# Kernel tuning notes

Hardware: AMD Instinct MI355X
Metric: run time of the kernel (lower is better)

The kernel has to match this reference:

```python
import jax, jax.numpy as jnp
import numpy as np

N = 20000      # num nodes
E = 320000     # num edges (avg degree 16)
R = 8          # num relations
D = 256        # input_dim / hidden dim
L = 6          # num_layers
EE = 32        # edge_embed_dim
B = 64         # batch size
K = 32         # num_negative + 1


def _layer_norm(x, g, b, eps=1e-5):
    mu = jnp.mean(x, axis=-1, keepdims=True)
    var = jnp.var(x, axis=-1, keepdims=True)
    return (x - mu) * jax.lax.rsqrt(var + eps) * g + b


def setup_inputs() -> dict:
    key = jax.random.key(0)
    ks = jax.random.split(key, 10)
    edge_index = jax.random.randint(ks[0], (2, E), 0, N)
    edge_type = jax.random.randint(ks[1], (E,), 0, R)
    edge_embed = jax.random.normal(ks[2], (E, EE), dtype=jnp.float32)
    src = jax.random.randint(ks[3], (B, K), 0, N)
    tgt = jax.random.randint(ks[4], (B, K), 0, N)
    rel = jax.random.randint(ks[5], (B, K), 0, R)
    batch = jnp.stack([src, tgt, rel], axis=-1)  # [B, K, 3]
    s = 1.0 / np.sqrt(D)
    W = jax.random.normal(ks[6], (L, R, D, D), dtype=jnp.float32) * s      # per-relation weights
    Wself = jax.random.normal(ks[7], (L, D, D), dtype=jnp.float32) * s     # self-loop weights
    We = jax.random.normal(ks[8], (L, EE, D), dtype=jnp.float32) * (1.0 / np.sqrt(EE))  # edge-embed proj (stage add)
    gamma = jnp.ones((L, D), dtype=jnp.float32)
    beta = jnp.zeros((L, D), dtype=jnp.float32)
    rel_emb = jax.random.normal(ks[9], (R, D), dtype=jnp.float32) * s      # DistMult relation embedding
    return dict(edge_index=edge_index, edge_type=edge_type, edge_embed=edge_embed,
                batch=batch, W=W, Wself=Wself, We=We, gamma=gamma, beta=beta,
                rel_emb=rel_emb)


def reference(edge_index, edge_type, edge_embed, batch, W, Wself, We, gamma, beta, rel_emb):
    src, dst = edge_index[0], edge_index[1]
    # mean aggregation denominator: in-degree per node (over all relations)
    deg = jnp.clip(jax.ops.segment_sum(jnp.ones((E,), jnp.float32), dst, num_segments=N), 1.0)
    # segment id combining relation and destination node -> aggregate-then-transform trick
    seg = edge_type * N + dst
    x = jnp.ones((N, D), dtype=jnp.float32)
    for l in range(L):
        # stage 'add': message = x[src] + proj(edge_embed)
        msg = x[src] + edge_embed @ We[l]                                  # [E, D]
        agg = jax.ops.segment_sum(msg, seg, num_segments=R * N).reshape(R, N, D)
        h = jnp.einsum('rnd,rdf->nf', agg, W[l]) / deg[:, None] + x @ Wself[l]
        h = jax.nn.relu(_layer_norm(h, gamma[l], beta[l]))
        x = h + x  # short_cut residual
    # DistMult scoring: gather source/target/relation embeddings, mul, sum
    s_emb = x[batch[..., 0]]          # [B, K, D]
    t_emb = x[batch[..., 1]]          # [B, K, D]
    r_emb = rel_emb[batch[..., 2]]    # [B, K, D]
    return jnp.sum(s_emb * r_emb * t_emb, axis=-1)  # [B, K]
```

## Files before the change

kernel.cpp:

```cpp
#include <hip/hip_runtime.h>
#include <hip/hip_bf16.h>

#define NN 20000
#define NP 20080
#define NE 320000
#define RR 8
#define DD 256
#define LL 6
#define EED 32
#define BB 64
#define KK 32
#define MM (NN * RR)
#define NSB 79
#define BMR 80
#define NGB 251

typedef __bf16 bf8 __attribute__((ext_vector_type(8)));
typedef float f4 __attribute__((ext_vector_type(4)));

__device__ inline float lo2f(unsigned v) { return __uint_as_float(v << 16); }
__device__ inline float hi2f(unsigned v) { return __uint_as_float(v & 0xffff0000u); }
__device__ inline unsigned short f2bf(float f) {
    unsigned u = __float_as_uint(f);
    return (unsigned short)((u + 0x7fff + ((u >> 16) & 1)) >> 16);
}
__device__ inline unsigned pack2(float lo, float hi) {
    return (unsigned)f2bf(lo) | ((unsigned)f2bf(hi) << 16);
}

#define GLOAD_LDS16(src, dst)                                                  \
    __builtin_amdgcn_global_load_lds(                                          \
        (const __attribute__((address_space(1))) unsigned int*)(src),          \
        (__attribute__((address_space(3))) unsigned int*)(dst), 16, 0, 0)


__global__ __launch_bounds__(256) void hist_kernel(const int* __restrict__ dstv,
                                                   const int* __restrict__ typev,
                                                   int* __restrict__ hist) {
    int e = blockIdx.x * 256 + threadIdx.x;
    if (e < NE) atomicAdd(&hist[dstv[e] * 8 + typev[e]], 1);
}

__global__ __launch_bounds__(256) void scan1_kernel(const int* __restrict__ hist,
                                                    int* __restrict__ excl,
                                                    int* __restrict__ bsums) {
    __shared__ int tmp[256];
    int tid = threadIdx.x;
    int base = blockIdx.x * 2048 + tid * 8;
    int v[8]; int s = 0;
#pragma unroll
    for (int i = 0; i < 8; ++i) {
        v[i] = (base + i < MM) ? hist[base + i] : 0;
        s += v[i];
    }
    tmp[tid] = s;
    __syncthreads();
    for (int off = 1; off < 256; off <<= 1) {
        int t = (tid >= off) ? tmp[tid - off] : 0;
        __syncthreads();
        tmp[tid] += t;
        __syncthreads();
    }
    int run = tmp[tid] - s;
#pragma unroll
    for (int i = 0; i < 8; ++i) {
        if (base + i < MM) excl[base + i] = run;
        run += v[i];
    }
    if (tid == 255) bsums[blockIdx.x] = tmp[255];
}

__global__ __launch_bounds__(128) void scan2_kernel(int* __restrict__ bsums) {
    __shared__ int tmp[128];
    int tid = threadIdx.x;
    int orig = (tid < NSB) ? bsums[tid] : 0;
    tmp[tid] = orig;
    __syncthreads();
    for (int off = 1; off < 128; off <<= 1) {
        int t = (tid >= off) ? tmp[tid - off] : 0;
        __syncthreads();
        tmp[tid] += t;
        __syncthreads();
    }
    if (tid < NSB) bsums[tid] = tmp[tid] - orig;
}

__global__ __launch_bounds__(256) void add_off_kernel(const int* __restrict__ excl,
                                                      const int* __restrict__ bsums,
                                                      int* __restrict__ seg_start,
                                                      int* __restrict__ cursor) {
    int i = blockIdx.x * 256 + threadIdx.x;
    if (i < MM) {
        int v = excl[i] + bsums[i >> 11];
        seg_start[i] = v;
        cursor[i] = v;
    }
    if (i == 0) seg_start[MM] = NE;
}

__global__ __launch_bounds__(256) void sort_scatter_kernel(
    const int* __restrict__ srcv, const int* __restrict__ dstv,
    const int* __restrict__ typev, int* __restrict__ cursor,
    int* __restrict__ esrc, int* __restrict__ eid) {
    int e = blockIdx.x * 256 + threadIdx.x;
    if (e < NE) {
        int key = dstv[e] * 8 + typev[e];
        int pos = atomicAdd(&cursor[key], 1);
        esrc[pos] = srcv[e];
        eid[pos]  = e;
    }
}

__global__ __launch_bounds__(256) void invdeg_kernel(const int* __restrict__ seg_start,
                                                     float* __restrict__ invdeg) {
    int i = blockIdx.x * 256 + threadIdx.x;
    if (i < NN) {
        int d = seg_start[i * 8 + 8] - seg_start[i * 8];
        invdeg[i] = 1.0f / (float)max(d, 1);
    }
}


__global__ __launch_bounds__(256) void eagg_kernel(
    const int* __restrict__ seg_start, const int* __restrict__ eid,
    const float* __restrict__ ee, const float* __restrict__ invdeg,
    unsigned short* __restrict__ eaggbf) {
    int tid = threadIdx.x;
    int s = blockIdx.x * 8 + (tid >> 5);
    int j = tid & 31;
    int n = s >> 3, r = s & 7;
    int j0 = seg_start[s], j1 = seg_start[s + 1];
    float sum = 0.0f;
    for (int p = j0; p < j1; ++p)
        sum += ee[eid[p] * EED + j];
    eaggbf[(size_t)n * DD + r * EED + j] = f2bf(sum * invdeg[n]);
}

__global__ __launch_bounds__(256) void whe_kernel(const float* __restrict__ We,
                                                  const float* __restrict__ W,
                                                  float* __restrict__ Whe) {
    __shared__ float WeS[EED * 32];
    int b = blockIdx.x;
    int l = b >> 6;
    int r = (b >> 3) & 7;
    int dc = b & 7;
    int tid = threadIdx.x;
    {
        int j = tid >> 3, dl = (tid & 7) * 4;
        *(float4*)&WeS[j * 32 + dl] =
            *(const float4*)&We[(size_t)l * EED * DD + (size_t)j * DD + dc * 32 + dl];
    }
    __syncthreads();
    const float* Wr = W + ((size_t)l * 8 + r) * DD * DD + (size_t)dc * 32 * DD;
    float acc[EED];
#pragma unroll
    for (int j = 0; j < EED; ++j) acc[j] = 0.0f;
    for (int dl = 0; dl < 32; ++dl) {
        float w = Wr[(size_t)dl * DD + tid];
#pragma unroll
        for (int j = 0; j < EED; ++j) acc[j] += WeS[j * 32 + dl] * w;
    }
    float* outp = Whe + (size_t)l * DD * DD + r * EED * DD + tid;
#pragma unroll
    for (int j = 0; j < EED; ++j) unsafeAtomicAdd(&outp[j * DD], acc[j]);
}

__global__ __launch_bounds__(256) void bswz_kernel(const float* __restrict__ W,
                                                   const float* __restrict__ Wself,
                                                   const float* __restrict__ Whe,
                                                   unsigned short* __restrict__ Bsw) {
    int gid = blockIdx.x * 256 + threadIdx.x;
    int f = gid & 255;
    int t = gid >> 8;
    int quad = t & 3; t >>= 2;
    int kb = t & 7; t >>= 3;
    int p = t % 10, l = t / 10;
    const float* base = (p == 0) ? Wself + (size_t)l * DD * DD
                      : (p <= 8) ? W + ((size_t)l * 8 + (p - 1)) * DD * DD
                                 : Whe + (size_t)l * DD * DD;
    int k0 = kb * 32 + quad * 8;
    unsigned pk[4];
#pragma unroll
    for (int jj = 0; jj < 4; ++jj)
        pk[jj] = pack2(base[(size_t)(k0 + 2 * jj) * DD + f],
                       base[(size_t)(k0 + 2 * jj + 1) * DD + f]);
    uint4 v = make_uint4(pk[0], pk[1], pk[2], pk[3]);
    *(uint4*)&Bsw[(size_t)gid * 8] = v;
}

__global__ __launch_bounds__(256) void init_x_kernel(float* __restrict__ x,
                                                     unsigned short* __restrict__ xbf) {
    int i = blockIdx.x * 256 + threadIdx.x;
    ((float4*)x)[i] = make_float4(1.f, 1.f, 1.f, 1.f);
    ((uint2*)xbf)[i] = make_uint2(0x3f803f80u, 0x3f803f80u);
}

__global__ __launch_bounds__(512) void agg_kernel(
    const int* __restrict__ seg_start, const int* __restrict__ esrc,
    const unsigned short* __restrict__ xbf, unsigned short* __restrict__ Abf) {
    int wv = threadIdx.x >> 6, lane = threadIdx.x & 63;
    int n = blockIdx.x * 8 + wv;
    if (n >= NN) return;
    int jb[9];
#pragma unroll
    for (int r = 0; r < 9; ++r) jb[r] = seg_start[n * 8 + r];
    float idg = 1.0f / (float)max(jb[8] - jb[0], 1);
    int cofs = lane * 4;
#pragma unroll
    for (int rr = 0; rr < 8; ++rr) {
        int j0 = jb[rr], j1 = jb[rr + 1];
        float a0 = 0.f, a1 = 0.f, a2 = 0.f, a3 = 0.f;
#pragma unroll 1
        for (int j = j0; j < j1; j += 8) {
            int rem = j1 - j;
            uint2 gvv[8];
#pragma unroll
            for (int t = 0; t < 8; ++t) {
                int jj = (t < rem) ? j + t : j;
                gvv[t] = *(const uint2*)&xbf[(size_t)esrc[jj] * DD + cofs];
            }
#pragma unroll
            for (int t = 0; t < 8; ++t) {
                unsigned vx = (t < rem) ? gvv[t].x : 0u;
                unsigned vy = (t < rem) ? gvv[t].y : 0u;
                a0 += lo2f(vx); a1 += hi2f(vx);
                a2 += lo2f(vy); a3 += hi2f(vy);
            }
        }
        *(uint2*)&Abf[(size_t)n * 2048 + rr * 256 + cofs] =
            make_uint2(pack2(a0 * idg, a1 * idg), pack2(a2 * idg, a3 * idg));
    }
}

__global__ __launch_bounds__(512) void gemm_layer_kernel(
    const unsigned short* __restrict__ xbfin, const unsigned short* __restrict__ Abf,
    const unsigned short* __restrict__ eaggbf, const unsigned short* __restrict__ Bswl,
    const float* __restrict__ xin, const float* __restrict__ gl,
    const float* __restrict__ bl, float* __restrict__ xout,
    unsigned short* __restrict__ xbfout) {
    __shared__ __align__(16) unsigned char smem[81920];
    int tid = threadIdx.x;
    int wv = tid >> 6, lane = tid & 63;
    int row0 = blockIdx.x * BMR;
    int m = lane & 15, quad = lane >> 4;
    f4 acc[5][2] = {};

#pragma unroll
    for (int i = 0; i < 5; ++i) {
        int bc = i * 512 + wv * 64;
        int c = bc + lane;
        int row = c >> 5, sc = c & 31, scs = sc ^ (row & 31);
        const unsigned short* src = xbfin + (size_t)(row0 + row) * DD + scs * 8;
        GLOAD_LDS16(src, smem + (size_t)bc * 16 + (size_t)lane * 16);
    }
    bf8 breg[2][2];
#pragma unroll
    for (int nt = 0; nt < 2; ++nt) {
        breg[0][nt] = *(const bf8*)&Bswl[((size_t)quad * 256 + wv * 32 + nt * 16 + m) * 8];
        breg[1][nt] = *(const bf8*)&Bswl[((size_t)(4 + quad) * 256 + wv * 32 + nt * 16 + m) * 8];
    }
    __syncthreads();

#pragma unroll 1
    for (int p = 0; p < 10; ++p) {
        unsigned char* bufp = smem + (p & 1) * 40960;
        unsigned char* bufn = smem + ((p + 1) & 1) * 40960;
        if (p < 9) {
            int q = p + 1;
            const unsigned short* sb;
            size_t rs;
            if (q <= 8) { sb = Abf + (size_t)row0 * 2048 + (size_t)(q - 1) * 256; rs = 2048; }
            else        { sb = eaggbf + (size_t)row0 * DD; rs = DD; }
#pragma unroll
            for (int i = 0; i < 5; ++i) {
                int bc = i * 512 + wv * 64;
                int c = bc + lane;
                int row = c >> 5, sc = c & 31, scs = sc ^ (row & 31);
                const unsigned short* src = sb + (size_t)row * rs + scs * 8;
                GLOAD_LDS16(src, bufn + (size_t)bc * 16 + (size_t)lane * 16);
            }
        }
#pragma unroll
        for (int kb = 0; kb < 8; ++kb) {
            bf8 afr[5];
#pragma unroll
            for (int mt = 0; mt < 5; ++mt) {
                int rowl = mt * 16 + m;
                afr[mt] = *(bf8*)&bufp[rowl * 512 + (((kb * 4 + quad) ^ (rowl & 31)) * 16)];
            }
#pragma unroll
            for (int mt = 0; mt < 5; ++mt)
#pragma unroll
                for (int nt = 0; nt < 2; ++nt)
                    acc[mt][nt] = __builtin_amdgcn_mfma_f32_16x16x32_bf16(
                        afr[mt], breg[kb & 1][nt], acc[mt][nt], 0, 0, 0);
            int gn = p * 8 + kb + 2;
            if (gn < 80) {
#pragma unroll
                for (int nt = 0; nt < 2; ++nt)
                    breg[kb & 1][nt] = *(const bf8*)&Bswl[((size_t)gn * 4 + quad) * 2048
                                                          + ((size_t)(wv * 32 + nt * 16 + m)) * 8];
            }
        }
        __syncthreads();
    }

    float* Hs = (float*)smem;
    float4 g  = *(const float4*)&gl[lane * 4];
    float4 bb = *(const float4*)&bl[lane * 4];
#pragma unroll
    for (int mt = 0; mt < 5; ++mt)
#pragma unroll
        for (int nt = 0; nt < 2; ++nt)
#pragma unroll
            for (int rg = 0; rg < 4; ++rg)
                Hs[(mt * 16 + quad * 4 + rg) * 256 + wv * 32 + nt * 16 + m] = acc[mt][nt][rg];
    __syncthreads();
#pragma unroll 1
    for (int rr = 0; rr < 10; ++rr) {
        int row = wv * 10 + rr;
        float4 v = *(float4*)&Hs[row * 256 + lane * 4];
        float s = v.x + v.y + v.z + v.w;
        float q = v.x * v.x + v.y * v.y + v.z * v.z + v.w * v.w;
#pragma unroll
        for (int off = 32; off; off >>= 1) {
            s += __shfl_xor(s, off);
            q += __shfl_xor(q, off);
        }
        float mu  = s * (1.0f / DD);
        float var = q * (1.0f / DD) - mu * mu;
        float rs  = rsqrtf(var + 1e-5f);
        size_t xi = (size_t)(row0 + row) * DD + lane * 4;
        float4 xv = *(const float4*)&xin[xi];
        float4 o;
        o.x = fmaxf((v.x - mu) * rs * g.x + bb.x, 0.0f) + xv.x;
        o.y = fmaxf((v.y - mu) * rs * g.y + bb.y, 0.0f) + xv.y;
        o.z = fmaxf((v.z - mu) * rs * g.z + bb.z, 0.0f) + xv.z;
        o.w = fmaxf((v.w - mu) * rs * g.w + bb.w, 0.0f) + xv.w;
        *(float4*)&xout[xi] = o;
        *(uint2*)&xbfout[xi] = make_uint2(pack2(o.x, o.y), pack2(o.z, o.w));
    }
}

__global__ __launch_bounds__(256) void score_kernel(
    const int* __restrict__ batch, const float* __restrict__ x,
    const float* __restrict__ rel_emb, float* __restrict__ out) {
    int tid = threadIdx.x;
    int wave = tid >> 6, lane = tid & 63;
    int idx = blockIdx.x * 4 + wave;
    int s = batch[idx * 3 + 0], t = batch[idx * 3 + 1], r = batch[idx * 3 + 2];
    float4 sv = *(const float4*)&x[(size_t)s * DD + lane * 4];
    float4 tv = *(const float4*)&x[(size_t)t * DD + lane * 4];
    float4 rv = *(const float4*)&rel_emb[(size_t)r * DD + lane * 4];
    float sum = sv.x * rv.x * tv.x + sv.y * rv.y * tv.y +
                sv.z * rv.z * tv.z + sv.w * rv.w * tv.w;
#pragma unroll
    for (int off = 32; off; off >>= 1) sum += __shfl_xor(sum, off);
    if (lane == 0) out[idx] = sum;
}

extern "C" void kernel_launch(void* const* d_in, const int* in_sizes, int n_in,
                              void* d_out, int out_size, void* d_ws, size_t ws_size,
                              hipStream_t stream) {
    const int*   edge_index = (const int*)d_in[0];
    const int*   srcv   = edge_index;
    const int*   dstv   = edge_index + NE;
    const int*   typev  = (const int*)d_in[1];
    const float* ee     = (const float*)d_in[2];
    const int*   batch  = (const int*)d_in[3];
    const float* W      = (const float*)d_in[4];
    const float* Wself  = (const float*)d_in[5];
    const float* We     = (const float*)d_in[6];
    const float* gamma  = (const float*)d_in[7];
    const float* beta   = (const float*)d_in[8];
    const float* rel_emb= (const float*)d_in[9];
    float* out = (float*)d_out;

    float* xA     = (float*)d_ws;
    float* xB     = xA + (size_t)NP * DD;
    float* Whe    = xB + (size_t)NP * DD;
    float* invdeg = Whe + (size_t)LL * DD * DD;
    unsigned short* xbfA   = (unsigned short*)(invdeg + NN);
    unsigned short* xbfB   = xbfA + (size_t)NP * DD;
    unsigned short* eaggbf = xbfB + (size_t)NP * DD;
    unsigned short* Bsw    = eaggbf + (size_t)NP * DD;
    int* hist      = (int*)(Bsw + (size_t)LL * 2560 * DD);
    int* excl      = hist + MM;
    int* seg_start = excl + MM;
    int* cursor    = seg_start + MM + 1;
    int* bsums     = cursor + MM;
    int* esrc      = bsums + 256;
    int* eid       = esrc + NE;
    unsigned short* Abf =
        (unsigned short*)(((uintptr_t)(eid + NE) + 255) & ~(uintptr_t)255);

    hipMemsetAsync(hist, 0, MM * sizeof(int), stream);
    hist_kernel<<<(NE + 255) / 256, 256, 0, stream>>>(dstv, typev, hist);
    scan1_kernel<<<NSB, 256, 0, stream>>>(hist, excl, bsums);
    scan2_kernel<<<1, 128, 0, stream>>>(bsums);
    add_off_kernel<<<(MM + 255) / 256, 256, 0, stream>>>(excl, bsums, seg_start, cursor);
    invdeg_kernel<<<(NN + 255) / 256, 256, 0, stream>>>(seg_start, invdeg);
    sort_scatter_kernel<<<(NE + 255) / 256, 256, 0, stream>>>(srcv, dstv, typev, cursor, esrc, eid);

    eagg_kernel<<<MM / 8, 256, 0, stream>>>(seg_start, eid, ee, invdeg, eaggbf);
    hipMemsetAsync(Whe, 0, (size_t)LL * DD * DD * sizeof(float), stream);
    whe_kernel<<<LL * 64, 256, 0, stream>>>(We, W, Whe);
    bswz_kernel<<<LL * 10 * 8 * 4, 256, 0, stream>>>(W, Wself, Whe, Bsw);
    init_x_kernel<<<(NP * DD / 4) / 256, 256, 0, stream>>>(xA, xbfA);

    float* xin = xA;  float* xout = xB;
    unsigned short* xbin = xbfA;  unsigned short* xbout = xbfB;
    for (int l = 0; l < LL; ++l) {
        agg_kernel<<<NP / 8, 512, 0, stream>>>(seg_start, esrc, xbin, Abf);
        gemm_layer_kernel<<<NGB, 512, 0, stream>>>(xbin, Abf, eaggbf,
            Bsw + (size_t)l * 2560 * DD, xin,
            gamma + (size_t)l * DD, beta + (size_t)l * DD, xout, xbout);
        float* t = xin; xin = xout; xout = t;
        unsigned short* tb = xbin; xbin = xbout; xbout = tb;
    }
    score_kernel<<<(BB * KK) / 4, 256, 0, stream>>>(batch, xin, rel_emb, out);
}
```

Baseline: 828.7 us.

## Switch to transform-then-aggregate with a per-relation projected Y and fused LayerNorm

Per layer, the layer first computes Y = x·[W_0..W_7, Wself] in bf16 for every node. It then gathers the relation-specific Y slice per edge, using precomputed byte offsets stored in the sorted edge list, and sums across all relations. The per-relation aggregate buffer and the 2560-deep GEMM go away, and LayerNorm, ReLU and the residual are fused into the gather kernel. The cost is a larger intermediate Y (about 2304 columns per node) that is written and then gathered randomly, with worse cache locality than gathering x. There is also an extra GEMM launch for the edge-embedding term, and the weights are now applied before the per-relation mean instead of after it, which adds bf16 rounding.

```diff
diff --git a/kernel.cpp b/kernel.cpp
--- a/kernel.cpp
+++ b/kernel.cpp
@@ -14,6 +14,8 @@
 #define NSB 79
 #define BMR 80
 #define NGB 251
+#define YROW 2304
+#define YROWB 4608
 
 typedef __bf16 bf8 __attribute__((ext_vector_type(8)));
 typedef float f4 __attribute__((ext_vector_type(4)));
@@ -101,13 +103,13 @@
 __global__ __launch_bounds__(256) void sort_scatter_kernel(
     const int* __restrict__ srcv, const int* __restrict__ dstv,
     const int* __restrict__ typev, int* __restrict__ cursor,
-    int* __restrict__ esrc, int* __restrict__ eid) {
+    int* __restrict__ esrcY, int* __restrict__ eid) {
     int e = blockIdx.x * 256 + threadIdx.x;
     if (e < NE) {
         int key = dstv[e] * 8 + typev[e];
         int pos = atomicAdd(&cursor[key], 1);
-        esrc[pos] = srcv[e];
-        eid[pos]  = e;
+        esrcY[pos] = srcv[e] * YROWB + typev[e] * 512;
+        eid[pos]   = e;
     }
 }
 
@@ -175,8 +177,8 @@
     int quad = t & 3; t >>= 2;
     int kb = t & 7; t >>= 3;
     int p = t % 10, l = t / 10;
-    const float* base = (p == 0) ? Wself + (size_t)l * DD * DD
-                      : (p <= 8) ? W + ((size_t)l * 8 + (p - 1)) * DD * DD
+    const float* base = (p <= 7) ? W + ((size_t)l * 8 + p) * DD * DD
+                      : (p == 8) ? Wself + (size_t)l * DD * DD
                                  : Whe + (size_t)l * DD * DD;
     int k0 = kb * 32 + quad * 8;
     unsigned pk[4];
@@ -188,105 +190,54 @@
     *(uint4*)&Bsw[(size_t)gid * 8] = v;
 }
 
-__global__ __launch_bounds__(256) void init_x_kernel(float* __restrict__ x,
-                                                     unsigned short* __restrict__ xbf) {
+__global__ __launch_bounds__(256) void init_x_kernel(float* __restrict__ xA,
+                                                     float* __restrict__ xB,
+                                                     unsigned short* __restrict__ xbfA,
+                                                     unsigned short* __restrict__ xbfB) {
     int i = blockIdx.x * 256 + threadIdx.x;
-    ((float4*)x)[i] = make_float4(1.f, 1.f, 1.f, 1.f);
-    ((uint2*)xbf)[i] = make_uint2(0x3f803f80u, 0x3f803f80u);
-}
-
-__global__ __launch_bounds__(512) void agg_kernel(
-    const int* __restrict__ seg_start, const int* __restrict__ esrc,
-    const unsigned short* __restrict__ xbf, unsigned short* __restrict__ Abf) {
-    int wv = threadIdx.x >> 6, lane = threadIdx.x & 63;
-    int n = blockIdx.x * 8 + wv;
-    if (n >= NN) return;
-    int jb[9];
-#pragma unroll
-    for (int r = 0; r < 9; ++r) jb[r] = seg_start[n * 8 + r];
-    float idg = 1.0f / (float)max(jb[8] - jb[0], 1);
-    int cofs = lane * 4;
-#pragma unroll
-    for (int rr = 0; rr < 8; ++rr) {
-        int j0 = jb[rr], j1 = jb[rr + 1];
-        float a0 = 0.f, a1 = 0.f, a2 = 0.f, a3 = 0.f;
-#pragma unroll 1
-        for (int j = j0; j < j1; j += 8) {
-            int rem = j1 - j;
-            uint2 gvv[8];
-#pragma unroll
-            for (int t = 0; t < 8; ++t) {
-                int jj = (t < rem) ? j + t : j;
-                gvv[t] = *(const uint2*)&xbf[(size_t)esrc[jj] * DD + cofs];
-            }
-#pragma unroll
-            for (int t = 0; t < 8; ++t) {
-                unsigned vx = (t < rem) ? gvv[t].x : 0u;
-                unsigned vy = (t < rem) ? gvv[t].y : 0u;
-                a0 += lo2f(vx); a1 += hi2f(vx);
-                a2 += lo2f(vy); a3 += hi2f(vy);
-            }
-        }
-        *(uint2*)&Abf[(size_t)n * 2048 + rr * 256 + cofs] =
-            make_uint2(pack2(a0 * idg, a1 * idg), pack2(a2 * idg, a3 * idg));
-    }
-}
-
-__global__ __launch_bounds__(512) void gemm_layer_kernel(
-    const unsigned short* __restrict__ xbfin, const unsigned short* __restrict__ Abf,
-    const unsigned short* __restrict__ eaggbf, const unsigned short* __restrict__ Bswl,
-    const float* __restrict__ xin, const float* __restrict__ gl,
-    const float* __restrict__ bl, float* __restrict__ xout,
-    unsigned short* __restrict__ xbfout) {
-    __shared__ __align__(16) unsigned char smem[81920];
+    ((float4*)xA)[i] = make_float4(1.f, 1.f, 1.f, 1.f);
+    ((float4*)xB)[i] = make_float4(1.f, 1.f, 1.f, 1.f);
+    ((uint2*)xbfA)[i] = make_uint2(0x3f803f80u, 0x3f803f80u);
+    ((uint2*)xbfB)[i] = make_uint2(0x3f803f80u, 0x3f803f80u);
+}
+
+__global__ __launch_bounds__(512) void ymm_kernel(
+    const unsigned short* __restrict__ Asrc, const unsigned short* __restrict__ Bswl,
+    unsigned short* __restrict__ Yout, int rtBeg, int rtEnd, int ostride) {
+    __shared__ __align__(16) unsigned char smem[40960 + 81920];
+    unsigned char* As = smem;
+    float* Hs = (float*)(smem + 40960);
     int tid = threadIdx.x;
     int wv = tid >> 6, lane = tid & 63;
     int row0 = blockIdx.x * BMR;
     int m = lane & 15, quad = lane >> 4;
-    f4 acc[5][2] = {};
 
 #pragma unroll
     for (int i = 0; i < 5; ++i) {
         int bc = i * 512 + wv * 64;
         int c = bc + lane;
         int row = c >> 5, sc = c & 31, scs = sc ^ (row & 31);
-        const unsigned short* src = xbfin + (size_t)(row0 + row) * DD + scs * 8;
-        GLOAD_LDS16(src, smem + (size_t)bc * 16 + (size_t)lane * 16);
-    }
+        GLOAD_LDS16(Asrc + (size_t)(row0 + row) * DD + scs * 8, As + (size_t)c * 16);
+    }
+    int gn0 = rtBeg * 8, gnEnd = rtEnd * 8;
     bf8 breg[2][2];
 #pragma unroll
     for (int nt = 0; nt < 2; ++nt) {
-        breg[0][nt] = *(const bf8*)&Bswl[((size_t)quad * 256 + wv * 32 + nt * 16 + m) * 8];
-        breg[1][nt] = *(const bf8*)&Bswl[((size_t)(4 + quad) * 256 + wv * 32 + nt * 16 + m) * 8];
+        breg[0][nt] = *(const bf8*)&Bswl[(((size_t)gn0 * 4 + quad) * 256 + wv * 32 + nt * 16 + m) * 8];
+        breg[1][nt] = *(const bf8*)&Bswl[(((size_t)(gn0 + 1) * 4 + quad) * 256 + wv * 32 + nt * 16 + m) * 8];
     }
     __syncthreads();
 
 #pragma unroll 1
-    for (int p = 0; p < 10; ++p) {
-        unsigned char* bufp = smem + (p & 1) * 40960;
-        unsigned char* bufn = smem + ((p + 1) & 1) * 40960;
-        if (p < 9) {
-            int q = p + 1;
-            const unsigned short* sb;
-            size_t rs;
-            if (q <= 8) { sb = Abf + (size_t)row0 * 2048 + (size_t)(q - 1) * 256; rs = 2048; }
-            else        { sb = eaggbf + (size_t)row0 * DD; rs = DD; }
-#pragma unroll
-            for (int i = 0; i < 5; ++i) {
-                int bc = i * 512 + wv * 64;
-                int c = bc + lane;
-                int row = c >> 5, sc = c & 31, scs = sc ^ (row & 31);
-                const unsigned short* src = sb + (size_t)row * rs + scs * 8;
-                GLOAD_LDS16(src, bufn + (size_t)bc * 16 + (size_t)lane * 16);
-            }
-        }
+    for (int rt = rtBeg; rt < rtEnd; ++rt) {
+        f4 acc[5][2] = {};
 #pragma unroll
         for (int kb = 0; kb < 8; ++kb) {
             bf8 afr[5];
 #pragma unroll
             for (int mt = 0; mt < 5; ++mt) {
                 int rowl = mt * 16 + m;
-                afr[mt] = *(bf8*)&bufp[rowl * 512 + (((kb * 4 + quad) ^ (rowl & 31)) * 16)];
+                afr[mt] = *(bf8*)&As[rowl * 512 + (((kb * 4 + quad) ^ (rowl & 31)) * 16)];
             }
 #pragma unroll
             for (int mt = 0; mt < 5; ++mt)
@@ -294,52 +245,93 @@
                 for (int nt = 0; nt < 2; ++nt)
                     acc[mt][nt] = __builtin_amdgcn_mfma_f32_16x16x32_bf16(
                         afr[mt], breg[kb & 1][nt], acc[mt][nt], 0, 0, 0);
-            int gn = p * 8 + kb + 2;
-            if (gn < 80) {
+            int gn = rt * 8 + kb + 2;
+            if (gn < gnEnd) {
 #pragma unroll
                 for (int nt = 0; nt < 2; ++nt)
                     breg[kb & 1][nt] = *(const bf8*)&Bswl[((size_t)gn * 4 + quad) * 2048
                                                           + ((size_t)(wv * 32 + nt * 16 + m)) * 8];
             }
         }
-        __syncthreads();
-    }
-
-    float* Hs = (float*)smem;
+#pragma unroll
+        for (int mt = 0; mt < 5; ++mt)
+#pragma unroll
+            for (int nt = 0; nt < 2; ++nt)
+#pragma unroll
+                for (int rg = 0; rg < 4; ++rg)
+                    Hs[(mt * 16 + quad * 4 + rg) * 256 + wv * 32 + nt * 16 + m] = acc[mt][nt][rg];
+        __syncthreads();
+        int colOff = (rt - rtBeg) * 256;
+#pragma unroll
+        for (int c2 = 0; c2 < 10; ++c2) {
+            int li = c2 * 512 + tid;
+            int row = li >> 6, u4 = li & 63;
+            float4 v = *(float4*)&Hs[row * 256 + u4 * 4];
+            *(uint2*)&Yout[(size_t)(row0 + row) * ostride + colOff + u4 * 4] =
+                make_uint2(pack2(v.x, v.y), pack2(v.z, v.w));
+        }
+        __syncthreads();
+    }
+}
+
+__global__ __launch_bounds__(512) void aggln_kernel(
+    const int* __restrict__ seg_start, const int* __restrict__ esrcY,
+    const unsigned short* __restrict__ Y, const unsigned short* __restrict__ eterml,
+    const float* __restrict__ xin, const float* __restrict__ gl,
+    const float* __restrict__ bl, float* __restrict__ xout,
+    unsigned short* __restrict__ xbfout) {
+    int tid = threadIdx.x;
+    int wv = tid >> 6, lane = tid & 63;
+    int n = blockIdx.x * 8 + wv;
     float4 g  = *(const float4*)&gl[lane * 4];
     float4 bb = *(const float4*)&bl[lane * 4];
-#pragma unroll
-    for (int mt = 0; mt < 5; ++mt)
-#pragma unroll
-        for (int nt = 0; nt < 2; ++nt)
-#pragma unroll
-            for (int rg = 0; rg < 4; ++rg)
-                Hs[(mt * 16 + quad * 4 + rg) * 256 + wv * 32 + nt * 16 + m] = acc[mt][nt][rg];
-    __syncthreads();
+    int j0 = seg_start[n * 8], j1 = seg_start[n * 8 + 8];
+    float idg = 1.0f / (float)max(j1 - j0, 1);
+    const char* Yb = (const char*)Y;
+    size_t lo8 = (size_t)(lane * 8);
+    float a0 = 0.f, a1 = 0.f, a2 = 0.f, a3 = 0.f;
 #pragma unroll 1
-    for (int rr = 0; rr < 10; ++rr) {
-        int row = wv * 10 + rr;
-        float4 v = *(float4*)&Hs[row * 256 + lane * 4];
-        float s = v.x + v.y + v.z + v.w;
-        float q = v.x * v.x + v.y * v.y + v.z * v.z + v.w * v.w;
-#pragma unroll
-        for (int off = 32; off; off >>= 1) {
-            s += __shfl_xor(s, off);
-            q += __shfl_xor(q, off);
+    for (int j = j0; j < j1; j += 8) {
+        int rem = j1 - j;
+        uint2 gvv[8];
+#pragma unroll
+        for (int t = 0; t < 8; ++t) {
+            int jj = (t < rem) ? j + t : j;
+            gvv[t] = *(const uint2*)(Yb + (size_t)(unsigned)esrcY[jj] + lo8);
         }
-        float mu  = s * (1.0f / DD);
-        float var = q * (1.0f / DD) - mu * mu;
-        float rs  = rsqrtf(var + 1e-5f);
-        size_t xi = (size_t)(row0 + row) * DD + lane * 4;
-        float4 xv = *(const float4*)&xin[xi];
-        float4 o;
-        o.x = fmaxf((v.x - mu) * rs * g.x + bb.x, 0.0f) + xv.x;
-        o.y = fmaxf((v.y - mu) * rs * g.y + bb.y, 0.0f) + xv.y;
-        o.z = fmaxf((v.z - mu) * rs * g.z + bb.z, 0.0f) + xv.z;
-        o.w = fmaxf((v.w - mu) * rs * g.w + bb.w, 0.0f) + xv.w;
-        *(float4*)&xout[xi] = o;
-        *(uint2*)&xbfout[xi] = make_uint2(pack2(o.x, o.y), pack2(o.z, o.w));
-    }
+#pragma unroll
+        for (int t = 0; t < 8; ++t) {
+            unsigned vx = (t < rem) ? gvv[t].x : 0u;
+            unsigned vy = (t < rem) ? gvv[t].y : 0u;
+            a0 += lo2f(vx); a1 += hi2f(vx);
+            a2 += lo2f(vy); a3 += hi2f(vy);
+        }
+    }
+    uint2 sv = *(const uint2*)(Yb + (size_t)n * YROWB + 4096 + lo8);
+    uint2 ev = *(const uint2*)&eterml[(size_t)n * DD + lane * 4];
+    float h0 = a0 * idg + lo2f(sv.x) + lo2f(ev.x);
+    float h1 = a1 * idg + hi2f(sv.x) + hi2f(ev.x);
+    float h2 = a2 * idg + lo2f(sv.y) + lo2f(ev.y);
+    float h3 = a3 * idg + hi2f(sv.y) + hi2f(ev.y);
+    float s = h0 + h1 + h2 + h3;
+    float q = h0 * h0 + h1 * h1 + h2 * h2 + h3 * h3;
+#pragma unroll
+    for (int off = 32; off; off >>= 1) {
+        s += __shfl_xor(s, off);
+        q += __shfl_xor(q, off);
+    }
+    float mu  = s * (1.0f / DD);
+    float var = q * (1.0f / DD) - mu * mu;
+    float rs  = rsqrtf(var + 1e-5f);
+    size_t xi = (size_t)n * DD + lane * 4;
+    float4 xv = *(const float4*)&xin[xi];
+    float4 o;
+    o.x = fmaxf((h0 - mu) * rs * g.x + bb.x, 0.0f) + xv.x;
+    o.y = fmaxf((h1 - mu) * rs * g.y + bb.y, 0.0f) + xv.y;
+    o.z = fmaxf((h2 - mu) * rs * g.z + bb.z, 0.0f) + xv.z;
+    o.w = fmaxf((h3 - mu) * rs * g.w + bb.w, 0.0f) + xv.w;
+    *(float4*)&xout[xi] = o;
+    *(uint2*)&xbfout[xi] = make_uint2(pack2(o.x, o.y), pack2(o.z, o.w));
 }
 
 __global__ __launch_bounds__(256) void score_kernel(
@@ -389,10 +381,11 @@
     int* seg_start = excl + MM;
     int* cursor    = seg_start + MM + 1;
     int* bsums     = cursor + MM;
-    int* esrc      = bsums + 256;
-    int* eid       = esrc + NE;
-    unsigned short* Abf =
+    int* esrcY     = bsums + 256;
+    int* eid       = esrcY + NE;
+    unsigned short* etermb =
         (unsigned short*)(((uintptr_t)(eid + NE) + 255) & ~(uintptr_t)255);
+    unsigned short* Y = etermb + (size_t)NP * DD;
 
     hipMemsetAsync(hist, 0, MM * sizeof(int), stream);
     hist_kernel<<<(NE + 255) / 256, 256, 0, stream>>>(dstv, typev, hist);
@@ -400,21 +393,22 @@
     scan2_kernel<<<1, 128, 0, stream>>>(bsums);
     add_off_kernel<<<(MM + 255) / 256, 256, 0, stream>>>(excl, bsums, seg_start, cursor);
     invdeg_kernel<<<(NN + 255) / 256, 256, 0, stream>>>(seg_start, invdeg);
-    sort_scatter_kernel<<<(NE + 255) / 256, 256, 0, stream>>>(srcv, dstv, typev, cursor, esrc, eid);
+    sort_scatter_kernel<<<(NE + 255) / 256, 256, 0, stream>>>(srcv, dstv, typev, cursor, esrcY, eid);
 
     eagg_kernel<<<MM / 8, 256, 0, stream>>>(seg_start, eid, ee, invdeg, eaggbf);
     hipMemsetAsync(Whe, 0, (size_t)LL * DD * DD * sizeof(float), stream);
     whe_kernel<<<LL * 64, 256, 0, stream>>>(We, W, Whe);
     bswz_kernel<<<LL * 10 * 8 * 4, 256, 0, stream>>>(W, Wself, Whe, Bsw);
-    init_x_kernel<<<(NP * DD / 4) / 256, 256, 0, stream>>>(xA, xbfA);
+    init_x_kernel<<<(NP * DD / 4) / 256, 256, 0, stream>>>(xA, xB, xbfA, xbfB);
 
     float* xin = xA;  float* xout = xB;
     unsigned short* xbin = xbfA;  unsigned short* xbout = xbfB;
     for (int l = 0; l < LL; ++l) {
-        agg_kernel<<<NP / 8, 512, 0, stream>>>(seg_start, esrc, xbin, Abf);
-        gemm_layer_kernel<<<NGB, 512, 0, stream>>>(xbin, Abf, eaggbf,
-            Bsw + (size_t)l * 2560 * DD, xin,
-            gamma + (size_t)l * DD, beta + (size_t)l * DD, xout, xbout);
+        const unsigned short* Bl = Bsw + (size_t)l * 2560 * DD;
+        ymm_kernel<<<NGB, 512, 0, stream>>>(xbin, Bl, Y, 0, 9, YROW);
+        ymm_kernel<<<NGB, 512, 0, stream>>>(eaggbf, Bl, etermb, 9, 10, DD);
+        aggln_kernel<<<NN / 8, 512, 0, stream>>>(seg_start, esrcY, Y, etermb,
+            xin, gamma + (size_t)l * DD, beta + (size_t)l * DD, xout, xbout);
         float* t = xin; xin = xout; xout = t;
         unsigned short* tb = xbin; xbin = xbout; xbout = tb;
     }
```

Result: faster. 755.6 us (-8.8%).
